# Optimization experiments

Measured on AMD Instinct MI355X. Metric: run time of the kernel, lower is better.

Reference implementation:

```python
import jax, jax.numpy as jnp
import numpy as np

HEADS = 4
DIM_HEAD = 32
SCALE = DIM_HEAD ** -0.5


def setup_inputs() -> dict:
    key = jax.random.key(0)
    k1, k2, k3 = jax.random.split(key, 3)
    B, C, H, W = 4, 128, 64, 64
    inner = HEADS * DIM_HEAD  # 128
    x = jax.random.normal(k1, (B, C, H, W), dtype=jnp.float32)
    # 1x1 conv weights == channel-mixing matrices [out_ch, in_ch]
    w_qkv = jax.random.normal(k2, (inner * 3, C), dtype=jnp.float32) * (C ** -0.5)
    w_proj = jax.random.normal(k3, (C, inner), dtype=jnp.float32) * (inner ** -0.5)
    b_proj = jnp.zeros((C,), dtype=jnp.float32)
    return {"x": x, "w_qkv": w_qkv, "w_proj": w_proj, "b_proj": b_proj}


def reference(x, w_qkv, w_proj, b_proj):
    b, c, h, w = x.shape
    n = h * w
    # 1x1 conv = per-pixel matmul over channels
    qkv = jnp.einsum('bchw,oc->bohw', x, w_qkv)  # [B, 3*inner, H, W]
    q, k, v = jnp.split(qkv, 3, axis=1)

    def to_heads(t):
        # [B, inner, H, W] -> [B, heads, HW, dim_head]
        return t.reshape(b, HEADS, DIM_HEAD, n).transpose(0, 1, 3, 2)

    q = to_heads(q) * SCALE
    k = to_heads(k)
    v = to_heads(v)
    # scores [B, heads, HW, HW]; softmax is max-stabilized (matches torch amax-subtract)
    scores = jnp.einsum('bhnd,bhmd->bhnm', q, k)
    attn = jax.nn.softmax(scores, axis=-1)
    out = jnp.einsum('bhnm,bhmd->bhnd', attn, v)  # [B, heads, HW, dim_head]
    out = out.transpose(0, 1, 3, 2).reshape(b, HEADS * DIM_HEAD, h, w)
    return jnp.einsum('bchw,oc->bohw', out, w_proj) + b_proj[None, :, None, None]
```

## Files before the change

kernel.cpp:

```cpp
#include <hip/hip_runtime.h>

typedef _Float16 f16;
typedef __attribute__((ext_vector_type(8))) f16 f16x8;
typedef __attribute__((ext_vector_type(4))) f16 f16x4;
typedef __attribute__((ext_vector_type(2))) __fp16 h16x2;
typedef __attribute__((ext_vector_type(4))) float floatx4;

#define NPIX 4096
#define KT   128
#define VROW 136

__global__ __launch_bounds__(256) void cvt_w(
    const float* __restrict__ wq, const float* __restrict__ wp,
    f16* __restrict__ wh, f16* __restrict__ wph)
{
    const int idx = (blockIdx.x * 256 + threadIdx.x) * 4;
    const float qs = 0.17677669529663687f * 1.4426950408889634f;
    float4 v;
    f16* dst;
    if (idx < 49152) { v = *(const float4*)(wq + idx); dst = wh + idx; }
    else             { v = *(const float4*)(wp + (idx - 49152)); dst = wph + (idx - 49152); }
    if (idx < 16384) { v.x *= qs; v.y *= qs; v.z *= qs; v.w *= qs; }
    h16x2 a = __builtin_amdgcn_cvt_pkrtz(v.x, v.y);
    h16x2 b = __builtin_amdgcn_cvt_pkrtz(v.z, v.w);
    f16x4 h; h[0] = (f16)a[0]; h[1] = (f16)a[1]; h[2] = (f16)b[0]; h[3] = (f16)b[1];
    *(f16x4*)dst = h;
}

__global__ __launch_bounds__(256) void qkv_mfma(
    const float* __restrict__ x, const f16* __restrict__ wh,
    f16* __restrict__ qh, f16* __restrict__ kh, f16* __restrict__ vth)
{
    const int tid  = threadIdx.x;
    const int wave = tid >> 6;
    const int lane = tid & 63;
    const int quad = lane >> 4;
    const int l16  = lane & 15;
    const int pbase = blockIdx.x * 64;
    const int y     = blockIdx.y;
    const int b     = blockIdx.z;
    const int p_col = pbase + wave * 16 + l16;

    const float* xb = x + (size_t)b * 128 * NPIX;

    f16x8 xf[4];
#pragma unroll
    for (int kc = 0; kc < 4; ++kc) {
        const int c0 = kc * 32 + quad * 8;
        float e[8];
#pragma unroll
        for (int j = 0; j < 8; ++j)
            e[j] = xb[(size_t)(c0 + j) * NPIX + p_col];
#pragma unroll
        for (int j = 0; j < 4; ++j) {
            h16x2 pk = __builtin_amdgcn_cvt_pkrtz(e[2 * j], e[2 * j + 1]);
            xf[kc][2 * j] = (f16)pk[0]; xf[kc][2 * j + 1] = (f16)pk[1];
        }
    }

    floatx4 acc[4];
#pragma unroll
    for (int i = 0; i < 4; ++i) acc[i] = floatx4{0.f, 0.f, 0.f, 0.f};

    if (y < 4) {
#pragma unroll
        for (int n = 0; n < 4; ++n)
#pragma unroll
            for (int kc = 0; kc < 4; ++kc) {
                f16x8 wf = *(const f16x8*)&wh[(size_t)(y * 64 + n * 16 + l16) * 128 + kc * 32 + quad * 8];
                acc[n] = __builtin_amdgcn_mfma_f32_16x16x32_f16(xf[kc], wf, acc[n], 0, 0, 0);
            }
        f16* dst = (y < 2) ? qh : kh;
#pragma unroll
        for (int n = 0; n < 4; ++n) {
            const int og    = y * 64 + n * 16 + l16;
            const int local = og & 127;
            const int head  = local >> 5;
            const int d     = local & 31;
            f16* base = dst + (size_t)(b * 4 + head) * NPIX * 32;
#pragma unroll
            for (int r = 0; r < 4; ++r) {
                const int p = pbase + wave * 16 + quad * 4 + r;
                base[(size_t)p * 32 + d] = (f16)acc[n][r];
            }
        }
    } else {
#pragma unroll
        for (int m = 0; m < 4; ++m)
#pragma unroll
            for (int kc = 0; kc < 4; ++kc) {
                f16x8 wf = *(const f16x8*)&wh[(size_t)(y * 64 + m * 16 + l16) * 128 + kc * 32 + quad * 8];
                acc[m] = __builtin_amdgcn_mfma_f32_16x16x32_f16(wf, xf[kc], acc[m], 0, 0, 0);
            }
#pragma unroll
        for (int m = 0; m < 4; ++m)
#pragma unroll
            for (int r = 0; r < 4; ++r) {
                const int ov   = (y - 4) * 64 + m * 16 + quad * 4 + r;
                const int head = ov >> 5;
                const int d    = ov & 31;
                vth[((size_t)(b * 4 + head) * 32 + d) * NPIX + p_col] = (f16)acc[m][r];
            }
    }
}

__global__ __launch_bounds__(256, 4) void attn_kernel(
    const f16* __restrict__ qh, const f16* __restrict__ kh,
    const f16* __restrict__ vth, f16* __restrict__ po, float* __restrict__ pl)
{
    __shared__ f16 klds[KT * 32];
    __shared__ f16 vlds[32 * VROW];

    const int tid  = threadIdx.x;
    const int wave = tid >> 6;
    const int lane = tid & 63;
    const int quad = lane >> 4;
    const int l16  = lane & 15;

    const int n     = blockIdx.x;
    const int bh    = (n & 7) * 2 + ((n >> 3) & 1);
    const int qblk  = (n >> 4) & 31;
    const int split = n >> 9;
    const int qbase = qblk * 128 + wave * 32;

    const f16* kb = kh + (size_t)bh * NPIX * 32;
    const f16* vb = vth + (size_t)bh * 32 * NPIX;

    f16x8 qB[2];
#pragma unroll
    for (int h = 0; h < 2; ++h)
        qB[h] = *(const f16x8*)(qh + ((size_t)bh * NPIX + qbase + h * 16 + l16) * 32 + quad * 8);

    floatx4 oacc[2][2];
#pragma unroll
    for (int h = 0; h < 2; ++h)
#pragma unroll
        for (int dh = 0; dh < 2; ++dh) oacc[h][dh] = floatx4{0.f, 0.f, 0.f, 0.f};
    float lsum[2] = {0.f, 0.f};

    for (int kt = split * 16; kt < split * 16 + 16; ++kt) {
        __syncthreads();
        {
            const int4* src = (const int4*)(kb + (size_t)kt * KT * 32);
            ((int4*)klds)[tid]       = src[tid];
            ((int4*)klds)[tid + 256] = src[tid + 256];
        }
        {
            const int r  = tid >> 3;
            const int cc = (tid & 7) * 2;
            const int4* vsrc = (const int4*)(vb + (size_t)r * NPIX + kt * KT + cc * 8);
            int4 v0 = vsrc[0], v1 = vsrc[1];
            int4* vdst = (int4*)(vlds + r * VROW + cc * 8);
            vdst[0] = v0; vdst[1] = v1;
        }
        __syncthreads();

        f16x8 kf[8];
#pragma unroll
        for (int t = 0; t < 8; ++t)
            kf[t] = *(const f16x8*)&klds[(t * 16 + l16) * 32 + quad * 8];

#pragma unroll
        for (int h = 0; h < 2; ++h) {
            floatx4 st[8];
#pragma unroll
            for (int t = 0; t < 8; ++t) {
                floatx4 z = {0.f, 0.f, 0.f, 0.f};
                st[t] = __builtin_amdgcn_mfma_f32_16x16x32_f16(kf[t], qB[h], z, 0, 0, 0);
            }
            f16x4 paf[8];
            float ls = 0.f;
#pragma unroll
            for (int t = 0; t < 8; ++t) {
                float e0 = __builtin_amdgcn_exp2f(st[t][0]);
                float e1 = __builtin_amdgcn_exp2f(st[t][1]);
                float e2 = __builtin_amdgcn_exp2f(st[t][2]);
                float e3 = __builtin_amdgcn_exp2f(st[t][3]);
                ls += (e0 + e1) + (e2 + e3);
                h16x2 lo = __builtin_amdgcn_cvt_pkrtz(e0, e1);
                h16x2 hi = __builtin_amdgcn_cvt_pkrtz(e2, e3);
                paf[t][0] = (f16)lo[0]; paf[t][1] = (f16)lo[1];
                paf[t][2] = (f16)hi[0]; paf[t][3] = (f16)hi[1];
            }
            lsum[h] += ls;
#pragma unroll
            for (int g = 0; g < 4; ++g) {
                f16x8 pA;
#pragma unroll
                for (int j = 0; j < 4; ++j) { pA[j] = paf[2 * g][j]; pA[4 + j] = paf[2 * g + 1][j]; }
#pragma unroll
                for (int dh = 0; dh < 2; ++dh) {
                    const f16* vrow = &vlds[(dh * 16 + l16) * VROW + 32 * g + quad * 4];
                    f16x4 v0 = *(const f16x4*)(vrow);
                    f16x4 v1 = *(const f16x4*)(vrow + 16);
                    f16x8 vB;
#pragma unroll
                    for (int j = 0; j < 4; ++j) { vB[j] = v0[j]; vB[4 + j] = v1[j]; }
                    oacc[h][dh] = __builtin_amdgcn_mfma_f32_16x16x32_f16(pA, vB, oacc[h][dh], 0, 0, 0);
                }
            }
        }
    }

    const size_t bq = (size_t)(split * 16 + bh) * NPIX;
#pragma unroll
    for (int h = 0; h < 2; ++h) {
        float l = lsum[h];
        l += __shfl_xor(l, 16);
        l += __shfl_xor(l, 32);
        if (quad == 0)
            pl[bq + qbase + h * 16 + l16] = l;
        f16* poh = po + (bq + qbase + h * 16) * 32;
#pragma unroll
        for (int r = 0; r < 4; ++r) {
            poh[(quad * 4 + r) * 32 + l16]      = (f16)oacc[h][0][r];
            poh[(quad * 4 + r) * 32 + 16 + l16] = (f16)oacc[h][1][r];
        }
    }
}

__global__ __launch_bounds__(256) void combine(
    const f16* __restrict__ po, const float* __restrict__ pl,
    f16* __restrict__ att)
{
    const int idx = blockIdx.x * 256 + threadIdx.x;
    const int qg  = idx >> 2;
    const int dg  = (idx & 3) * 8;
    const size_t sstride = (size_t)16 * NPIX * 32;

    f16x8 a = *(const f16x8*)(po + (size_t)qg * 32 + dg);
    f16x8 b = *(const f16x8*)(po + sstride + (size_t)qg * 32 + dg);
    const float inv = 1.0f / (pl[qg] + pl[qg + 16 * NPIX]);
    f16x8 o;
#pragma unroll
    for (int j = 0; j < 8; ++j)
        o[j] = (f16)(((float)a[j] + (float)b[j]) * inv);
    *(f16x8*)(att + (size_t)qg * 32 + dg) = o;
}

__global__ __launch_bounds__(256) void proj_mfma(
    const f16* __restrict__ att, const f16* __restrict__ wph,
    const float* __restrict__ bp, float* __restrict__ out)
{
    const int tid  = threadIdx.x;
    const int wave = tid >> 6;
    const int lane = tid & 63;
    const int quad = lane >> 4;
    const int l16  = lane & 15;
    const int pbase = blockIdx.x * 64;
    const int obase = blockIdx.y * 64;
    const int b     = blockIdx.z;
    const int p_col = pbase + wave * 16 + l16;

    const f16* ab = att + (size_t)b * 4 * NPIX * 32;
    f16x8 bf[4];
#pragma unroll
    for (int kc = 0; kc < 4; ++kc)
        bf[kc] = *(const f16x8*)(ab + ((size_t)kc * NPIX + p_col) * 32 + quad * 8);

    floatx4 acc[4];
#pragma unroll
    for (int m = 0; m < 4; ++m) acc[m] = floatx4{0.f, 0.f, 0.f, 0.f};
#pragma unroll
    for (int m = 0; m < 4; ++m)
#pragma unroll
        for (int kc = 0; kc < 4; ++kc) {
            f16x8 af = *(const f16x8*)&wph[(size_t)(obase + m * 16 + l16) * 128 + kc * 32 + quad * 8];
            acc[m] = __builtin_amdgcn_mfma_f32_16x16x32_f16(af, bf[kc], acc[m], 0, 0, 0);
        }

#pragma unroll
    for (int m = 0; m < 4; ++m)
#pragma unroll
        for (int r = 0; r < 4; ++r) {
            const int o = obase + m * 16 + quad * 4 + r;
            out[((size_t)b * 128 + o) * NPIX + p_col] = acc[m][r] + bp[o];
        }
}

extern "C" void kernel_launch(void* const* d_in, const int* in_sizes, int n_in,
                              void* d_out, int out_size, void* d_ws, size_t ws_size,
                              hipStream_t stream)
{
    const float* x      = (const float*)d_in[0];
    const float* w_qkv  = (const float*)d_in[1];
    const float* w_proj = (const float*)d_in[2];
    const float* b_proj = (const float*)d_in[3];
    float* out = (float*)d_out;

    char* ws = (char*)d_ws;
    f16*   qh  = (f16*)(ws);
    f16*   kh  = (f16*)(ws + (4u << 20));
    f16*   vth = (f16*)(ws + (8u << 20));
    f16*   att = (f16*)(ws + (12u << 20));
    f16*   wh  = (f16*)(ws + (16u << 20));
    f16*   wph = (f16*)(ws + (16u << 20) + (96u << 10));
    float* pl  = (float*)(ws + (16u << 20) + (128u << 10));
    f16*   po  = (f16*)(ws + (17u << 20));

    cvt_w<<<dim3(64, 1, 1), 256, 0, stream>>>(w_qkv, w_proj, wh, wph);
    qkv_mfma<<<dim3(64, 6, 4), 256, 0, stream>>>(x, wh, qh, kh, vth);
    attn_kernel<<<dim3(1024, 1, 1), 256, 0, stream>>>(qh, kh, vth, po, pl);
    combine<<<dim3(1024, 1, 1), 256, 0, stream>>>(po, pl, att);
    proj_mfma<<<dim3(64, 2, 4), 256, 0, stream>>>(att, wph, b_proj, out);
}
```

Before: 141.5 us.

## Split attention KV into four chunks, fuse combine into projection, MFMA row sums

Doubles the KV split count so each attention block handles half as many key tiles and launches twice as many blocks. The separate combine kernel is removed; the projection kernel now reduces the four partial outputs and row sums itself before its MFMA. Row sums of the exponentiated scores are computed with an extra MFMA against a one-hot ones vector instead of VALU adds and cross-lane shuffles. This trades extra partial-output traffic and redundant reduction work in the projection for fewer launches and less VALU work in the attention inner loop.

```diff
diff --git a/kernel.cpp b/kernel.cpp
--- a/kernel.cpp
+++ b/kernel.cpp
@@ -9,6 +9,7 @@
 #define NPIX 4096
 #define KT   128
 #define VROW 136
+#define NSPLIT 4
 
 __global__ __launch_bounds__(256) void cvt_w(
     const float* __restrict__ wq, const float* __restrict__ wp,
@@ -120,7 +121,7 @@
     const int n     = blockIdx.x;
     const int bh    = (n & 7) * 2 + ((n >> 3) & 1);
     const int qblk  = (n >> 4) & 31;
-    const int split = n >> 9;
+    const int split = (n >> 9) & 3;
     const int qbase = qblk * 128 + wave * 32;
 
     const f16* kb = kh + (size_t)bh * NPIX * 32;
@@ -131,14 +132,19 @@
     for (int h = 0; h < 2; ++h)
         qB[h] = *(const f16x8*)(qh + ((size_t)bh * NPIX + qbase + h * 16 + l16) * 32 + quad * 8);
 
-    floatx4 oacc[2][2];
-#pragma unroll
-    for (int h = 0; h < 2; ++h)
+    f16x8 ones;
+#pragma unroll
+    for (int j = 0; j < 8; ++j) ones[j] = (l16 == 0) ? (f16)1.0f : (f16)0.0f;
+
+    floatx4 oacc[2][2], lacc[2];
+#pragma unroll
+    for (int h = 0; h < 2; ++h) {
+        lacc[h] = floatx4{0.f, 0.f, 0.f, 0.f};
 #pragma unroll
         for (int dh = 0; dh < 2; ++dh) oacc[h][dh] = floatx4{0.f, 0.f, 0.f, 0.f};
-    float lsum[2] = {0.f, 0.f};
-
-    for (int kt = split * 16; kt < split * 16 + 16; ++kt) {
+    }
+
+    for (int kt = split * 8; kt < split * 8 + 8; ++kt) {
         __syncthreads();
         {
             const int4* src = (const int4*)(kb + (size_t)kt * KT * 32);
@@ -163,31 +169,29 @@
 #pragma unroll
         for (int h = 0; h < 2; ++h) {
             floatx4 st[8];
-#pragma unroll
-            for (int t = 0; t < 8; ++t) {
-                floatx4 z = {0.f, 0.f, 0.f, 0.f};
-                st[t] = __builtin_amdgcn_mfma_f32_16x16x32_f16(kf[t], qB[h], z, 0, 0, 0);
-            }
+            const floatx4 z0 = {0.f, 0.f, 0.f, 0.f};
+#pragma unroll
+            for (int t = 0; t < 8; ++t)
+                st[t] = __builtin_amdgcn_mfma_f32_16x16x32_f16(kf[t], qB[h], z0, 0, 0, 0);
+
             f16x4 paf[8];
-            float ls = 0.f;
 #pragma unroll
             for (int t = 0; t < 8; ++t) {
                 float e0 = __builtin_amdgcn_exp2f(st[t][0]);
                 float e1 = __builtin_amdgcn_exp2f(st[t][1]);
                 float e2 = __builtin_amdgcn_exp2f(st[t][2]);
                 float e3 = __builtin_amdgcn_exp2f(st[t][3]);
-                ls += (e0 + e1) + (e2 + e3);
                 h16x2 lo = __builtin_amdgcn_cvt_pkrtz(e0, e1);
                 h16x2 hi = __builtin_amdgcn_cvt_pkrtz(e2, e3);
                 paf[t][0] = (f16)lo[0]; paf[t][1] = (f16)lo[1];
                 paf[t][2] = (f16)hi[0]; paf[t][3] = (f16)hi[1];
             }
-            lsum[h] += ls;
 #pragma unroll
             for (int g = 0; g < 4; ++g) {
                 f16x8 pA;
 #pragma unroll
                 for (int j = 0; j < 4; ++j) { pA[j] = paf[2 * g][j]; pA[4 + j] = paf[2 * g + 1][j]; }
+                lacc[h] = __builtin_amdgcn_mfma_f32_16x16x32_f16(pA, ones, lacc[h], 0, 0, 0);
 #pragma unroll
                 for (int dh = 0; dh < 2; ++dh) {
                     const f16* vrow = &vlds[(dh * 16 + l16) * VROW + 32 * g + quad * 4];
@@ -205,11 +209,11 @@
     const size_t bq = (size_t)(split * 16 + bh) * NPIX;
 #pragma unroll
     for (int h = 0; h < 2; ++h) {
-        float l = lsum[h];
-        l += __shfl_xor(l, 16);
-        l += __shfl_xor(l, 32);
-        if (quad == 0)
-            pl[bq + qbase + h * 16 + l16] = l;
+        if (l16 == 0) {
+#pragma unroll
+            for (int r = 0; r < 4; ++r)
+                pl[bq + qbase + h * 16 + quad * 4 + r] = lacc[h][r];
+        }
         f16* poh = po + (bq + qbase + h * 16) * 32;
 #pragma unroll
         for (int r = 0; r < 4; ++r) {
@@ -219,28 +223,10 @@
     }
 }
 
-__global__ __launch_bounds__(256) void combine(
+__global__ __launch_bounds__(256) void proj_mfma(
     const f16* __restrict__ po, const float* __restrict__ pl,
-    f16* __restrict__ att)
-{
-    const int idx = blockIdx.x * 256 + threadIdx.x;
-    const int qg  = idx >> 2;
-    const int dg  = (idx & 3) * 8;
-    const size_t sstride = (size_t)16 * NPIX * 32;
-
-    f16x8 a = *(const f16x8*)(po + (size_t)qg * 32 + dg);
-    f16x8 b = *(const f16x8*)(po + sstride + (size_t)qg * 32 + dg);
-    const float inv = 1.0f / (pl[qg] + pl[qg + 16 * NPIX]);
-    f16x8 o;
-#pragma unroll
-    for (int j = 0; j < 8; ++j)
-        o[j] = (f16)(((float)a[j] + (float)b[j]) * inv);
-    *(f16x8*)(att + (size_t)qg * 32 + dg) = o;
-}
-
-__global__ __launch_bounds__(256) void proj_mfma(
-    const f16* __restrict__ att, const f16* __restrict__ wph,
-    const float* __restrict__ bp, float* __restrict__ out)
+    const f16* __restrict__ wph, const float* __restrict__ bp,
+    float* __restrict__ out)
 {
     const int tid  = threadIdx.x;
     const int wave = tid >> 6;
@@ -252,11 +238,27 @@
     const int b     = blockIdx.z;
     const int p_col = pbase + wave * 16 + l16;
 
-    const f16* ab = att + (size_t)b * 4 * NPIX * 32;
     f16x8 bf[4];
 #pragma unroll
-    for (int kc = 0; kc < 4; ++kc)
-        bf[kc] = *(const f16x8*)(ab + ((size_t)kc * NPIX + p_col) * 32 + quad * 8);
+    for (int kc = 0; kc < 4; ++kc) {
+        const int bh = b * 4 + kc;
+        float sums[8] = {0.f, 0.f, 0.f, 0.f, 0.f, 0.f, 0.f, 0.f};
+        float lt = 0.f;
+#pragma unroll
+        for (int s = 0; s < NSPLIT; ++s) {
+            const size_t bq = (size_t)(s * 16 + bh) * NPIX + p_col;
+            f16x8 a = *(const f16x8*)(po + bq * 32 + quad * 8);
+#pragma unroll
+            for (int j = 0; j < 8; ++j) sums[j] += (float)a[j];
+            lt += pl[bq];
+        }
+        const float inv = 1.0f / lt;
+#pragma unroll
+        for (int j = 0; j < 4; ++j) {
+            h16x2 pk = __builtin_amdgcn_cvt_pkrtz(sums[2 * j] * inv, sums[2 * j + 1] * inv);
+            bf[kc][2 * j] = (f16)pk[0]; bf[kc][2 * j + 1] = (f16)pk[1];
+        }
+    }
 
     floatx4 acc[4];
 #pragma unroll
@@ -292,15 +294,13 @@
     f16*   qh  = (f16*)(ws);
     f16*   kh  = (f16*)(ws + (4u << 20));
     f16*   vth = (f16*)(ws + (8u << 20));
-    f16*   att = (f16*)(ws + (12u << 20));
-    f16*   wh  = (f16*)(ws + (16u << 20));
-    f16*   wph = (f16*)(ws + (16u << 20) + (96u << 10));
-    float* pl  = (float*)(ws + (16u << 20) + (128u << 10));
-    f16*   po  = (f16*)(ws + (17u << 20));
+    f16*   wh  = (f16*)(ws + (12u << 20));
+    f16*   wph = (f16*)(ws + (12u << 20) + (96u << 10));
+    float* pl  = (float*)(ws + (12u << 20) + (128u << 10));
+    f16*   po  = (f16*)(ws + (13u << 20) + (128u << 10));
 
     cvt_w<<<dim3(64, 1, 1), 256, 0, stream>>>(w_qkv, w_proj, wh, wph);
     qkv_mfma<<<dim3(64, 6, 4), 256, 0, stream>>>(x, wh, qh, kh, vth);
-    attn_kernel<<<dim3(1024, 1, 1), 256, 0, stream>>>(qh, kh, vth, po, pl);
-    combine<<<dim3(1024, 1, 1), 256, 0, stream>>>(po, pl, att);
-    proj_mfma<<<dim3(64, 2, 4), 256, 0, stream>>>(att, wph, b_proj, out);
-}
+    attn_kernel<<<dim3(2048, 1, 1), 256, 0, stream>>>(qh, kh, vth, po, pl);
+    proj_mfma<<<dim3(64, 2, 4), 256, 0, stream>>>(po, pl, wph, b_proj, out);
+}
```

New measurement: 141.5 us. About the same (+0.1%).
